# Kernel tuning notes

Hardware: AMD Instinct MI355X
Metric: run time of the kernel (lower is better)

## Reference

```python
import jax, jax.numpy as jnp
import numpy as np

B, J, D = 512, 22, 3
HIDDEN = 512
OUT = J * D          # 66, flattened frame size
NCLS = 12
LENGTH = 64


def setup_inputs() -> dict:
    key = jax.random.key(0)
    ks = jax.random.split(key, 12)
    s = 0.05
    return {
        "inputs": jax.random.normal(ks[0], (B, J, D), dtype=jnp.float32),
        "labels": jax.random.randint(ks[1], (B,), 0, NCLS),
        "length": LENGTH,
        # LSTMCell params (torch layout: W_ih [4H, in], W_hh [4H, H], gate order i,f,g,o)
        "W_ih": jax.random.normal(ks[2], (4 * HIDDEN, OUT + NCLS), dtype=jnp.float32) * s,
        "W_hh": jax.random.normal(ks[3], (4 * HIDDEN, HIDDEN), dtype=jnp.float32) * s,
        "b_ih": jax.random.normal(ks[4], (4 * HIDDEN,), dtype=jnp.float32) * s,
        "b_hh": jax.random.normal(ks[5], (4 * HIDDEN,), dtype=jnp.float32) * s,
        # fc: hidden -> output
        "W_fc": jax.random.normal(ks[6], (OUT, HIDDEN), dtype=jnp.float32) * s,
        "b_fc": jax.random.normal(ks[7], (OUT,), dtype=jnp.float32) * s,
        # fc_inh / fc_inc: output -> hidden (initial state projections)
        "W_inh": jax.random.normal(ks[8], (HIDDEN, OUT), dtype=jnp.float32) * s,
        "b_inh": jax.random.normal(ks[9], (HIDDEN,), dtype=jnp.float32) * s,
        "W_inc": jax.random.normal(ks[10], (HIDDEN, OUT), dtype=jnp.float32) * s,
        "b_inc": jax.random.normal(ks[11], (HIDDEN,), dtype=jnp.float32) * s,
    }


def reference(inputs, labels, length, W_ih, W_hh, b_ih, b_hh, W_fc, b_fc,
              W_inh, b_inh, W_inc, b_inc):
    b, j, d = inputs.shape
    enc = jax.nn.one_hot(labels, NCLS, dtype=inputs.dtype)      # [B, NCLS]
    frame0 = inputs.reshape(b, j * d)                            # [B, OUT]
    h0 = frame0 @ W_inh.T + b_inh                                # [B, H]
    c0 = frame0 @ W_inc.T + b_inc                                # [B, H]
    frame = jnp.concatenate([frame0, enc], axis=-1)              # [B, OUT+NCLS]

    def step(carry, _):
        h, c, fr = carry
        gates = fr @ W_ih.T + b_ih + h @ W_hh.T + b_hh           # [B, 4H]
        i, f, g, o = jnp.split(gates, 4, axis=-1)                # torch gate order
        c_new = jax.nn.sigmoid(f) * c + jax.nn.sigmoid(i) * jnp.tanh(g)
        h_new = jax.nn.sigmoid(o) * jnp.tanh(c_new)
        out = h_new @ W_fc.T + b_fc                              # [B, OUT]
        fr_new = jnp.concatenate([out, enc], axis=-1)
        return (h_new, c_new, fr_new), out

    _, outs = jax.lax.scan(step, (h0, c0, frame), None, length=length)  # [L, B, OUT]
    return jnp.transpose(outs, (1, 0, 2)).reshape(b, length, j, d)
```

## Files before the change

### kernel.cpp

```cpp
#include <hip/hip_runtime.h>

#define OUTD 66
#define INW  78
#define FH   2048
#define LEN  64

typedef short bf16x8 __attribute__((ext_vector_type(8)));
typedef float f32x4  __attribute__((ext_vector_type(4)));

__device__ __forceinline__ float bf2f(unsigned short u) {
  union { unsigned int i; float f; } v; v.i = ((unsigned int)u) << 16; return v.f;
}
__device__ __forceinline__ unsigned short f2bf(float f) {
  union { float f; unsigned int i; } v; v.f = f;
  unsigned int u = v.i;
  return (unsigned short)((u + 0x7fffu + ((u >> 16) & 1u)) >> 16);
}
__device__ __forceinline__ float sigm(float x) { return 1.f / (1.f + __expf(-x)); }
__device__ __forceinline__ float tanh_f(float x) { return 2.f / (1.f + __expf(-2.f * x)) - 1.f; }

__global__ __launch_bounds__(256) void k_initA(
    const float* __restrict__ W_hh, const float* __restrict__ W_ih,
    const float* __restrict__ W_fc, const float* __restrict__ b_ih,
    const float* __restrict__ b_hh, const float* __restrict__ b_fc,
    const float* __restrict__ inp, const float* __restrict__ W_inh,
    const float* __restrict__ b_inh, const float* __restrict__ W_inc,
    const float* __restrict__ b_inc,
    unsigned short* __restrict__ Weff, float* __restrict__ bias_eff,
    unsigned short* __restrict__ hbuf, float* __restrict__ c0,
    unsigned short* __restrict__ Wfc16, unsigned int* __restrict__ flags,
    unsigned int* __restrict__ flagsL)
{
  int tid = threadIdx.x, bid = blockIdx.x;
  if (bid < 256) {
    int nb = bid;
    int k = tid * 2;
    float acc[8][2];
    #pragma unroll
    for (int r = 0; r < 8; ++r) {
      int n = nb * 8 + r;
      acc[r][0] = W_hh[n * 512 + k];
      acc[r][1] = W_hh[n * 512 + k + 1];
    }
    for (int m = 0; m < OUTD; ++m) {
      float w0 = W_fc[m * 512 + k];
      float w1 = W_fc[m * 512 + k + 1];
      #pragma unroll
      for (int r = 0; r < 8; ++r) {
        float wih = W_ih[(nb * 8 + r) * INW + m];
        acc[r][0] += wih * w0;
        acc[r][1] += wih * w1;
      }
    }
    #pragma unroll
    for (int r = 0; r < 8; ++r) {
      int n = nb * 8 + r;
      unsigned int pack = (unsigned int)f2bf(acc[r][0]) | ((unsigned int)f2bf(acc[r][1]) << 16);
      *(unsigned int*)(Weff + n * 512 + k) = pack;
    }
    if (tid < 8) {
      int n = nb * 8 + tid;
      float a = b_ih[n] + b_hh[n];
      for (int m = 0; m < OUTD; ++m) a += b_fc[m] * W_ih[n * INW + m];
      bias_eff[n] = a;
    }
    if (nb == 0) {
      for (int i = tid; i < 512 * 16; i += 256) flags[i] = 0;
      for (int i = tid; i < 256 * 16; i += 256) flagsL[i] = 0;
    }
  } else {
    int nb = bid - 256;
    for (int r = 0; r < 2; ++r) {
      int b = nb * 2 + r;
      for (int half = 0; half < 2; ++half) {
        int c = tid + half * 256;
        float ha = b_inh[c], ca = b_inc[c];
        for (int m = 0; m < OUTD; ++m) {
          float f = inp[b * OUTD + m];
          ha += f * W_inh[c * OUTD + m];
          ca += f * W_inc[c * OUTD + m];
        }
        hbuf[b * 512 + c] = f2bf(ha);
        c0[b * 512 + c] = ca;
      }
    }
    if (nb == 0) {
      for (int i = tid; i < OUTD * 512; i += 256) Wfc16[i] = f2bf(W_fc[i]);
    }
  }
}

__global__ __launch_bounds__(128) void k_init2a(
    const float* __restrict__ inp, const unsigned short* __restrict__ hbuf,
    const float* __restrict__ W_fc, const float* __restrict__ b_fc,
    float* __restrict__ d0)
{
  int b = blockIdx.x, m = threadIdx.x;
  if (m >= OUTD) return;
  const unsigned short* hrow = hbuf + b * 512;
  const float* wrow = W_fc + m * 512;
  float acc = 0.f;
  for (int k = 0; k < 512; ++k) acc += bf2f(hrow[k]) * wrow[k];
  d0[b * OUTD + m] = inp[b * OUTD + m] - (acc + b_fc[m]);
}

__global__ __launch_bounds__(256) void k_init2b(
    const float* __restrict__ d0, const float* __restrict__ W_ih,
    float* __restrict__ corr0)
{
  __shared__ float ds[4][OUTD];
  int tid = threadIdx.x, b0 = blockIdx.x * 4;
  for (int i = tid; i < 4 * OUTD; i += 256) ds[i / OUTD][i % OUTD] = d0[b0 * OUTD + i];
  __syncthreads();
  for (int n = tid; n < FH; n += 256) {
    float a0 = 0, a1 = 0, a2 = 0, a3 = 0;
    const float* wr = W_ih + n * INW;
    for (int m = 0; m < OUTD; ++m) {
      float w = wr[m];
      a0 += ds[0][m] * w; a1 += ds[1][m] * w; a2 += ds[2][m] * w; a3 += ds[3][m] * w;
    }
    corr0[(b0 + 0) * FH + n] = a0;
    corr0[(b0 + 1) * FH + n] = a1;
    corr0[(b0 + 2) * FH + n] = a2;
    corr0[(b0 + 3) * FH + n] = a3;
  }
}

__global__ __launch_bounds__(256, 1) void k_main(
    const unsigned short* __restrict__ Weff, const float* __restrict__ bias_eff,
    unsigned short* __restrict__ hbuf, const float* __restrict__ c0,
    const float* __restrict__ corr0, const float* __restrict__ W_ih,
    const int* __restrict__ labels, const unsigned short* __restrict__ Wfc16,
    const float* __restrict__ b_fc, float* __restrict__ out,
    unsigned int* __restrict__ flags, unsigned int* __restrict__ flagsL)
{
  __shared__ __align__(16) unsigned short h_lds[64 * 512];

  int tid = threadIdx.x, bid = blockIdx.x;
  int w = tid >> 6, lane = tid & 63;
  int lc = lane & 15, kg = lane >> 4;
  unsigned int* xmap = flags + 4096;
  unsigned int* decp = flags + 4088;

  unsigned int xcd;
  asm volatile("s_getreg_b32 %0, hwreg(HW_REG_XCC_ID)" : "=s"(xcd));
  if (tid == 0)
    __hip_atomic_store(&xmap[bid * 16], xcd + 1u, __ATOMIC_RELAXED, __HIP_MEMORY_SCOPE_AGENT);

  if (bid == 0 && w == 0) {
    int okA = 1, okB = 1;
    #pragma unroll
    for (int i = 0; i < 4; ++i) {
      int b = lane + i * 64;
      unsigned int v, ra, rb;
      const unsigned int* xp = &xmap[b * 16];
      for (;;) { v = __hip_atomic_load(xp, __ATOMIC_RELAXED, __HIP_MEMORY_SCOPE_AGENT);
                 if (v) break; __builtin_amdgcn_s_sleep(1); }
      const unsigned int* pa = &xmap[(b & 7) * 16];
      for (;;) { ra = __hip_atomic_load(pa, __ATOMIC_RELAXED, __HIP_MEMORY_SCOPE_AGENT);
                 if (ra) break; __builtin_amdgcn_s_sleep(1); }
      const unsigned int* pb = &xmap[((b >> 5) << 5) * 16];
      for (;;) { rb = __hip_atomic_load(pb, __ATOMIC_RELAXED, __HIP_MEMORY_SCOPE_AGENT);
                 if (rb) break; __builtin_amdgcn_s_sleep(1); }
      okA &= (v == ra); okB &= (v == rb);
    }
    okA = __all(okA); okB = __all(okB);
    if (lane == 0) {
      unsigned int d = okA ? 1u : (okB ? 2u : 3u);
      __hip_atomic_store(decp, d, __ATOMIC_RELAXED, __HIP_MEMORY_SCOPE_AGENT);
    }
  }
  if (tid == 0) {
    unsigned int dd;
    for (;;) { dd = __hip_atomic_load(decp, __ATOMIC_RELAXED, __HIP_MEMORY_SCOPE_AGENT);
               if (dd) break; __builtin_amdgcn_s_sleep(1); }
    h_lds[0] = (unsigned short)dd;
  }
  __syncthreads();
  unsigned int dmode = h_lds[0];
  __syncthreads();

  int fast, mt, jt;
  if (dmode == 1u)      { fast = 1; mt = bid & 7;  jt = bid >> 3; }
  else if (dmode == 2u) { fast = 1; mt = bid >> 5; jt = bid & 31; }
  else                  { fast = 0; mt = bid & 7;  jt = bid >> 3; }

  int row0 = mt * 64, j0 = jt * 16;
  int hx0 = (w >> 1) * 8;
  int xloc = lc & 7;
  int G = lc >> 3;
  int hcol = j0 + hx0 + xloc;
  int rw0 = (w & 1) * 32;

  int sA = xloc;
  int tA16 = ((kg ^ sA) & 3) << 4;
  int ue64 = ((sA >> 2) & 1) << 6;
  int PA0 = (rw0 + lc) * 1024 + tA16 + ue64;
  int PA1 = PA0 + 16 * 1024;
  int PF  = (w * 16 + lc) * 1024 + tA16 + ue64;

  bf16x8 Bfrag[16][2];
  #pragma unroll
  for (int cg = 0; cg < 2; ++cg) {
    int n = (cg * 2 + G) * 512 + hcol;
    const unsigned short* p = Weff + n * 512 + kg * 8;
    #pragma unroll
    for (int i = 0; i < 16; ++i) Bfrag[i][cg] = *(const bf16x8*)(p + i * 32);
  }

  bf16x8 Wf[16];
  float fcb = 0.f;
  {
    int n = j0 + lc;
    if (jt < 5 && n < OUTD) {
      const unsigned short* p = Wfc16 + n * 512 + kg * 8;
      #pragma unroll
      for (int i = 0; i < 16; ++i) Wf[i] = *(const bf16x8*)(p + i * 32);
      fcb = b_fc[n];
    } else {
      bf16x8 z8 = {0, 0, 0, 0, 0, 0, 0, 0};
      #pragma unroll
      for (int i = 0; i < 16; ++i) Wf[i] = z8;
    }
  }

  int qsel = G * 2;
  float lt[4][4], creg[4];
  #pragma unroll
  for (int idx = 0; idx < 4; ++idx) {
    int rloc = rw0 + (idx >> 1) * 16 + kg * 4 + qsel + (idx & 1);
    int grow = row0 + rloc;
    int lab = labels[grow];
    #pragma unroll
    for (int gt = 0; gt < 4; ++gt) {
      int n = gt * 512 + hcol;
      lt[gt][idx] = bias_eff[n] + W_ih[n * INW + OUTD + lab];
    }
    creg[idx] = c0[grow * 512 + hcol];
  }

  const f32x4 z = {0.f, 0.f, 0.f, 0.f};
  unsigned int* myflag  = &flags[(mt * 32 + jt) * 16];
  unsigned int* myflagL = &flagsL[(mt * 32 + jt) * 16];
  const unsigned int* fpoll  = flags  + (mt * 32 + (lane & 31)) * 16;
  volatile const unsigned int* fpollL = flagsL + (mt * 32 + (lane & 31)) * 16;
  int useL = 1;

  for (int s = 0; s < LEN; ++s) {
    const unsigned short* hsrc = hbuf + (s & 1) * 262144 + row0 * 512;
    #pragma unroll
    for (int i = 0; i < 16; ++i) {
      int chunk = tid + i * 256;
      int r = chunk >> 6, g = chunk & 63;
      int dst = r * 512 + ((g ^ (r & 7)) << 3);
      *(uint4*)(h_lds + dst) = *(const uint4*)(hsrc + r * 512 + g * 8);
    }
    __syncthreads();

    f32x4 acc00 = z, acc01 = z, acc10 = z, acc11 = z;
    #pragma unroll
    for (int i = 0; i < 16; ++i) {
      bf16x8 a0 = *(const bf16x8*)((const char*)h_lds + (PA0 ^ (i << 6)));
      bf16x8 a1 = *(const bf16x8*)((const char*)h_lds + (PA1 ^ (i << 6)));
      acc00 = __builtin_amdgcn_mfma_f32_16x16x32_bf16(a0, Bfrag[i][0], acc00, 0, 0, 0);
      acc10 = __builtin_amdgcn_mfma_f32_16x16x32_bf16(a1, Bfrag[i][0], acc10, 0, 0, 0);
      acc01 = __builtin_amdgcn_mfma_f32_16x16x32_bf16(a0, Bfrag[i][1], acc01, 0, 0, 0);
      acc11 = __builtin_amdgcn_mfma_f32_16x16x32_bf16(a1, Bfrag[i][1], acc11, 0, 0, 0);
    }

    f32x4 sh00, sh01, sh10, sh11;
    #pragma unroll
    for (int j = 0; j < 4; ++j) {
      sh00[j] = __shfl_xor(acc00[j], 8);
      sh01[j] = __shfl_xor(acc01[j], 8);
      sh10[j] = __shfl_xor(acc10[j], 8);
      sh11[j] = __shfl_xor(acc11[j], 8);
    }

    unsigned short hval[4];
    #pragma unroll
    for (int idx = 0; idx < 4; ++idx) {
      int jj = idx & 1, hh = idx >> 1;
      int qo = qsel + jj;
      float xi, xf, xg, xo;
      if (hh == 0) {
        xi = (G ? sh00[qo] : acc00[qo]);
        xf = (G ? acc00[qo] : sh00[qo]);
        xg = (G ? sh01[qo] : acc01[qo]);
        xo = (G ? acc01[qo] : sh01[qo]);
      } else {
        xi = (G ? sh10[qo] : acc10[qo]);
        xf = (G ? acc10[qo] : sh10[qo]);
        xg = (G ? sh11[qo] : acc11[qo]);
        xo = (G ? acc11[qo] : sh11[qo]);
      }
      xi += lt[0][idx]; xf += lt[1][idx]; xg += lt[2][idx]; xo += lt[3][idx];
      if (s == 0) {
        int rloc = rw0 + hh * 16 + kg * 4 + qo;
        const float* cr = corr0 + (long)(row0 + rloc) * FH + hcol;
        xi += cr[0]; xf += cr[512]; xg += cr[1024]; xo += cr[1536];
      }
      float cn = sigm(xf) * creg[idx] + sigm(xi) * tanh_f(xg);
      creg[idx] = cn;
      hval[idx] = f2bf(sigm(xo) * tanh_f(cn));
    }

    {
      unsigned int* hdst32 = (unsigned int*)(hbuf + ((s + 1) & 1) * 262144);
      int ce = (hcol & ~1) >> 1;
      int odd = xloc & 1;
      unsigned int pk[2]; int ro[2]; int np = 0;
      #pragma unroll
      for (int idx = 0; idx < 4; ++idx) {
        unsigned int mine = hval[idx];
        unsigned int part = (unsigned int)__shfl_xor((int)mine, 1);
        unsigned int p = odd ? (part | (mine << 16)) : (mine | (part << 16));
        if ((idx >> 1) == odd) {
          int rloc = rw0 + (idx >> 1) * 16 + kg * 4 + qsel + (idx & 1);
          pk[np] = p; ro[np] = (row0 + rloc) * 256 + ce; ++np;
        }
      }
      if (fast) {
        hdst32[ro[0]] = pk[0];
        hdst32[ro[1]] = pk[1];
      } else {
        __hip_atomic_store(&hdst32[ro[0]], pk[0], __ATOMIC_RELAXED, __HIP_MEMORY_SCOPE_AGENT);
        __hip_atomic_store(&hdst32[ro[1]], pk[1], __ATOMIC_RELAXED, __HIP_MEMORY_SCOPE_AGENT);
      }
    }

    __builtin_amdgcn_s_waitcnt(0);
    __syncthreads();
    if (tid == 0) {
      if (fast) {
        *(volatile unsigned int*)myflagL = (unsigned int)(s + 1);
      }
      __hip_atomic_store(myflag, (unsigned int)(s + 1),
                         __ATOMIC_RELAXED, __HIP_MEMORY_SCOPE_AGENT);
    }

    if (jt < 5 && s >= 1) {
      f32x4 fa = z;
      #pragma unroll
      for (int i = 0; i < 16; ++i) {
        bf16x8 a = *(const bf16x8*)((const char*)h_lds + (PF ^ (i << 6)));
        fa = __builtin_amdgcn_mfma_f32_16x16x32_bf16(a, Wf[i], fa, 0, 0, 0);
      }
      int c = j0 + lc;
      if (c < OUTD) {
        #pragma unroll
        for (int q = 0; q < 4; ++q) {
          int b = row0 + w * 16 + kg * 4 + q;
          out[((long)b * 64 + (s - 1)) * OUTD + c] = fa[q] + fcb;
        }
      }
    }

    if (w == 0) {
      int done = 0;
      if (fast && useL) {
        for (int t = 0; t < 512; ++t) {
          asm volatile("buffer_inv\n\ts_waitcnt vmcnt(0)" ::: "memory");
          unsigned int v = *fpollL;
          if (__all((int)(v >= (unsigned int)(s + 1)))) { done = 1; break; }
        }
        if (!done) useL = 0;
      }
      if (!done) {
        for (;;) {
          unsigned int v = __hip_atomic_load(fpoll, __ATOMIC_RELAXED, __HIP_MEMORY_SCOPE_AGENT);
          if (__all((int)(v >= (unsigned int)(s + 1)))) break;
          __builtin_amdgcn_s_sleep(1);
        }
        __builtin_amdgcn_fence(__ATOMIC_ACQUIRE, "agent");
      }
    }
    __syncthreads();
  }

  if (jt < 5) {
    const unsigned short* hsrc = hbuf + row0 * 512;
    #pragma unroll
    for (int i = 0; i < 16; ++i) {
      int chunk = tid + i * 256;
      int r = chunk >> 6, g = chunk & 63;
      int dst = r * 512 + ((g ^ (r & 7)) << 3);
      *(uint4*)(h_lds + dst) = *(const uint4*)(hsrc + r * 512 + g * 8);
    }
    __syncthreads();
    f32x4 fa = z;
    #pragma unroll
    for (int i = 0; i < 16; ++i) {
      bf16x8 a = *(const bf16x8*)((const char*)h_lds + (PF ^ (i << 6)));
      fa = __builtin_amdgcn_mfma_f32_16x16x32_bf16(a, Wf[i], fa, 0, 0, 0);
    }
    int c = j0 + lc;
    if (c < OUTD) {
      #pragma unroll
      for (int q = 0; q < 4; ++q) {
        int b = row0 + w * 16 + kg * 4 + q;
        out[((long)b * 64 + 63) * OUTD + c] = fa[q] + fcb;
      }
    }
  }
}

extern "C" void kernel_launch(void* const* d_in, const int* in_sizes, int n_in,
                              void* d_out, int out_size, void* d_ws, size_t ws_size,
                              hipStream_t stream) {
  (void)in_sizes; (void)n_in; (void)out_size; (void)ws_size;
  const float* inp   = (const float*)d_in[0];
  const int*   labels= (const int*)d_in[1];
  const float* W_ih  = (const float*)d_in[3];
  const float* W_hh  = (const float*)d_in[4];
  const float* b_ih  = (const float*)d_in[5];
  const float* b_hh  = (const float*)d_in[6];
  const float* W_fc  = (const float*)d_in[7];
  const float* b_fc  = (const float*)d_in[8];
  const float* W_inh = (const float*)d_in[9];
  const float* b_inh = (const float*)d_in[10];
  const float* W_inc = (const float*)d_in[11];
  const float* b_inc = (const float*)d_in[12];

  char* ws = (char*)d_ws;
  unsigned short* Weff = (unsigned short*)(ws + 0);
  float* bias_eff      = (float*)(ws + 2097152);
  unsigned short* hbuf = (unsigned short*)(ws + 2105344);
  float* c0            = (float*)(ws + 3153920);
  float* corr0         = (float*)(ws + 4202496);
  float* d0            = (float*)(ws + 8396800);
  unsigned int* flags  = (unsigned int*)(ws + 8531968);
  unsigned short* Wfc16= (unsigned short*)(ws + 8564736);
  unsigned int* flagsL = (unsigned int*)(ws + 8632320);

  k_initA<<<512, 256, 0, stream>>>(W_hh, W_ih, W_fc, b_ih, b_hh, b_fc,
                                   inp, W_inh, b_inh, W_inc, b_inc,
                                   Weff, bias_eff, hbuf, c0, Wfc16, flags, flagsL);
  k_init2a<<<512, 128, 0, stream>>>(inp, hbuf, W_fc, b_fc, d0);
  k_init2b<<<128, 256, 0, stream>>>(d0, W_ih, corr0);

  k_main<<<256, 256, 0, stream>>>(Weff, bias_eff, hbuf, c0, corr0, W_ih, labels,
                                  Wfc16, b_fc, (float*)d_out, flags, flagsL);
}
```

Measured before the change: 501.1 us.

## Poll per-producer flags and fetch tiled h chunks as soon as each arrives

```diff
diff --git a/kernel.cpp b/kernel.cpp
--- a/kernel.cpp
+++ b/kernel.cpp
@@ -7,6 +7,7 @@
 
 typedef short bf16x8 __attribute__((ext_vector_type(8)));
 typedef float f32x4  __attribute__((ext_vector_type(4)));
+typedef unsigned int u32x4 __attribute__((ext_vector_type(4)));
 
 __device__ __forceinline__ float bf2f(unsigned short u) {
   union { unsigned int i; float f; } v; v.i = ((unsigned int)u) << 16; return v.f;
@@ -18,6 +19,13 @@
 }
 __device__ __forceinline__ float sigm(float x) { return 1.f / (1.f + __expf(-x)); }
 __device__ __forceinline__ float tanh_f(float x) { return 2.f / (1.f + __expf(-2.f * x)) - 1.f; }
+
+__device__ __forceinline__ unsigned int ld_flag_sc0(const unsigned int* p) {
+  unsigned int v;
+  asm volatile("global_load_dword %0, %1, off sc0\n\ts_waitcnt vmcnt(0)"
+               : "=v"(v) : "v"(p) : "memory");
+  return v;
+}
 
 __global__ __launch_bounds__(256) void k_initA(
     const float* __restrict__ W_hh, const float* __restrict__ W_ih,
@@ -80,7 +88,7 @@
           ha += f * W_inh[c * OUTD + m];
           ca += f * W_inc[c * OUTD + m];
         }
-        hbuf[b * 512 + c] = f2bf(ha);
+        hbuf[((b >> 6) * 32 + (c >> 4)) * 1024 + (b & 63) * 16 + (c & 15)] = f2bf(ha);
         c0[b * 512 + c] = ca;
       }
     }
@@ -97,10 +105,11 @@
 {
   int b = blockIdx.x, m = threadIdx.x;
   if (m >= OUTD) return;
-  const unsigned short* hrow = hbuf + b * 512;
+  const unsigned short* hb = hbuf + (b >> 6) * 32768 + (b & 63) * 16;
   const float* wrow = W_fc + m * 512;
   float acc = 0.f;
-  for (int k = 0; k < 512; ++k) acc += bf2f(hrow[k]) * wrow[k];
+  for (int k = 0; k < 512; ++k)
+    acc += bf2f(hb[(k >> 4) * 1024 + (k & 15)]) * wrow[k];
   d0[b * OUTD + m] = inp[b * OUTD + m] - (acc + b_fc[m]);
 }
 
@@ -135,6 +144,7 @@
     unsigned int* __restrict__ flags, unsigned int* __restrict__ flagsL)
 {
   __shared__ __align__(16) unsigned short h_lds[64 * 512];
+  (void)flagsL;
 
   int tid = threadIdx.x, bid = blockIdx.x;
   int w = tid >> 6, lane = tid & 63;
@@ -240,23 +250,23 @@
   }
 
   const f32x4 z = {0.f, 0.f, 0.f, 0.f};
-  unsigned int* myflag  = &flags[(mt * 32 + jt) * 16];
-  unsigned int* myflagL = &flagsL[(mt * 32 + jt) * 16];
-  const unsigned int* fpoll  = flags  + (mt * 32 + (lane & 31)) * 16;
-  volatile const unsigned int* fpollL = flagsL + (mt * 32 + (lane & 31)) * 16;
-  int useL = 1;
+  unsigned int* myflag = &flags[(mt * 32 + jt) * 16];
+  int scOk = 1;
+
+  {
+    const unsigned short* hsrc = hbuf + mt * 32768;
+    #pragma unroll
+    for (int i = 0; i < 16; ++i) {
+      int n = tid + i * 256;
+      int c = n >> 7, q = n & 127;
+      int r = q >> 1, u = q & 1, g = c * 2 + u;
+      *(u32x4*)(h_lds + r * 512 + ((g ^ (r & 7)) << 3)) =
+          *(const u32x4*)(hsrc + n * 8);
+    }
+  }
+  __syncthreads();
 
   for (int s = 0; s < LEN; ++s) {
-    const unsigned short* hsrc = hbuf + (s & 1) * 262144 + row0 * 512;
-    #pragma unroll
-    for (int i = 0; i < 16; ++i) {
-      int chunk = tid + i * 256;
-      int r = chunk >> 6, g = chunk & 63;
-      int dst = r * 512 + ((g ^ (r & 7)) << 3);
-      *(uint4*)(h_lds + dst) = *(const uint4*)(hsrc + r * 512 + g * 8);
-    }
-    __syncthreads();
-
     f32x4 acc00 = z, acc01 = z, acc10 = z, acc11 = z;
     #pragma unroll
     for (int i = 0; i < 16; ++i) {
@@ -307,7 +317,8 @@
 
     {
       unsigned int* hdst32 = (unsigned int*)(hbuf + ((s + 1) & 1) * 262144);
-      int ce = (hcol & ~1) >> 1;
+      int base32 = (mt * 32 + jt) * 512;
+      int ceL = (hx0 >> 1) + (xloc >> 1);
       int odd = xloc & 1;
       unsigned int pk[2]; int ro[2]; int np = 0;
       #pragma unroll
@@ -317,7 +328,7 @@
         unsigned int p = odd ? (part | (mine << 16)) : (mine | (part << 16));
         if ((idx >> 1) == odd) {
           int rloc = rw0 + (idx >> 1) * 16 + kg * 4 + qsel + (idx & 1);
-          pk[np] = p; ro[np] = (row0 + rloc) * 256 + ce; ++np;
+          pk[np] = p; ro[np] = base32 + rloc * 8 + ceL; ++np;
         }
       }
       if (fast) {
@@ -332,20 +343,81 @@
     __builtin_amdgcn_s_waitcnt(0);
     __syncthreads();
     if (tid == 0) {
-      if (fast) {
-        *(volatile unsigned int*)myflagL = (unsigned int)(s + 1);
-      }
-      __hip_atomic_store(myflag, (unsigned int)(s + 1),
-                         __ATOMIC_RELAXED, __HIP_MEMORY_SCOPE_AGENT);
-    }
-
-    if (jt < 5 && s >= 1) {
-      f32x4 fa = z;
+      if (fast)
+        *(volatile unsigned int*)myflag = (unsigned int)(s + 1);
+      else
+        __hip_atomic_store(myflag, (unsigned int)(s + 1),
+                           __ATOMIC_RELAXED, __HIP_MEMORY_SCOPE_AGENT);
+    }
+
+    f32x4 fa = z;
+    int dofc = (jt < 5) & (s >= 1);
+    if (dofc) {
       #pragma unroll
       for (int i = 0; i < 16; ++i) {
         bf16x8 a = *(const bf16x8*)((const char*)h_lds + (PF ^ (i << 6)));
         fa = __builtin_amdgcn_mfma_f32_16x16x32_bf16(a, Wf[i], fa, 0, 0, 0);
       }
+    }
+    __syncthreads();
+
+    if (s < LEN - 1 || jt < 5) {
+      const unsigned short* hbC = hbuf + ((s + 1) & 1) * 262144 + mt * 32768;
+      const unsigned int* fbase = flags + (mt * 32 + w * 8 + (lane & 7)) * 16;
+      unsigned int done = 0;
+      int it = 0;
+      while (done != 0xffu) {
+        unsigned int fv; int viaInv = 0;
+        if (fast) {
+          ++it;
+          if (!scOk || (it & 63) == 0) {
+            asm volatile("buffer_inv\n\ts_waitcnt vmcnt(0)" ::: "memory");
+            fv = *(volatile const unsigned int*)fbase;
+            viaInv = 1;
+          } else {
+            fv = ld_flag_sc0(fbase);
+          }
+        } else {
+          fv = __hip_atomic_load(fbase, __ATOMIC_RELAXED, __HIP_MEMORY_SCOPE_AGENT);
+        }
+        unsigned int todo =
+            ((unsigned int)__ballot(fv >= (unsigned int)(s + 1)) & 0xffu) & ~done;
+        if (!todo) { if (!fast) __builtin_amdgcn_s_sleep(1); continue; }
+        if (viaInv && it > 192) scOk = 0;
+        if (!fast) __builtin_amdgcn_fence(__ATOMIC_ACQUIRE, "agent");
+        int useSc0 = fast && !viaInv;
+
+        u32x4 ta[8], tb[8];
+        #pragma unroll
+        for (int i = 0; i < 8; ++i) {
+          if ((todo >> i) & 1u) {
+            const unsigned short* cp = hbC + (w * 8 + i) * 1024 + lane * 8;
+            if (useSc0) {
+              asm volatile("global_load_dwordx4 %0, %2, off sc0\n\t"
+                           "global_load_dwordx4 %1, %3, off sc0"
+                           : "=&v"(ta[i]), "=&v"(tb[i])
+                           : "v"(cp), "v"(cp + 512) : "memory");
+            } else {
+              ta[i] = *(const u32x4*)cp;
+              tb[i] = *(const u32x4*)(cp + 512);
+            }
+          }
+        }
+        if (useSc0) asm volatile("s_waitcnt vmcnt(0)" ::: "memory");
+        int r0 = lane >> 1, u = lane & 1, r1 = 32 + r0;
+        #pragma unroll
+        for (int i = 0; i < 8; ++i) {
+          if ((todo >> i) & 1u) {
+            int c2 = (w * 8 + i) * 2 + u;
+            *(u32x4*)(h_lds + r0 * 512 + ((c2 ^ (r0 & 7)) << 3)) = ta[i];
+            *(u32x4*)(h_lds + r1 * 512 + ((c2 ^ (r1 & 7)) << 3)) = tb[i];
+          }
+        }
+        done |= todo;
+      }
+    }
+
+    if (dofc) {
       int c = j0 + lc;
       if (c < OUTD) {
         #pragma unroll
@@ -355,39 +427,10 @@
         }
       }
     }
-
-    if (w == 0) {
-      int done = 0;
-      if (fast && useL) {
-        for (int t = 0; t < 512; ++t) {
-          asm volatile("buffer_inv\n\ts_waitcnt vmcnt(0)" ::: "memory");
-          unsigned int v = *fpollL;
-          if (__all((int)(v >= (unsigned int)(s + 1)))) { done = 1; break; }
-        }
-        if (!done) useL = 0;
-      }
-      if (!done) {
-        for (;;) {
-          unsigned int v = __hip_atomic_load(fpoll, __ATOMIC_RELAXED, __HIP_MEMORY_SCOPE_AGENT);
-          if (__all((int)(v >= (unsigned int)(s + 1)))) break;
-          __builtin_amdgcn_s_sleep(1);
-        }
-        __builtin_amdgcn_fence(__ATOMIC_ACQUIRE, "agent");
-      }
-    }
     __syncthreads();
   }
 
   if (jt < 5) {
-    const unsigned short* hsrc = hbuf + row0 * 512;
-    #pragma unroll
-    for (int i = 0; i < 16; ++i) {
-      int chunk = tid + i * 256;
-      int r = chunk >> 6, g = chunk & 63;
-      int dst = r * 512 + ((g ^ (r & 7)) << 3);
-      *(uint4*)(h_lds + dst) = *(const uint4*)(hsrc + r * 512 + g * 8);
-    }
-    __syncthreads();
     f32x4 fa = z;
     #pragma unroll
     for (int i = 0; i < 16; ++i) {
```

Result: slower. 1.856 ms (+270.3%).
